# Kernel tuning notes

Measured on AMD Instinct MI355X. Metric: run time of the kernel, lower is better.

Reference implementation:

```python
import jax, jax.numpy as jnp
import numpy as np

N_NODES = 100000
N_EDGES = 1600000
D_IN = 128
D_OUT = 128
SLOPE = 0.2


def setup_inputs() -> dict:
    key = jax.random.key(0)
    k1, k2, k3, k4 = jax.random.split(key, 4)
    x = jax.random.normal(k1, (N_NODES, D_IN), dtype=jnp.float32)
    edge_index = jax.random.randint(k2, (2, N_EDGES), 0, N_NODES, dtype=jnp.int64)
    scale = 1.0 / np.sqrt(D_IN)
    W_l = jax.random.normal(k3, (D_OUT, D_IN), dtype=jnp.float32) * scale
    b_l = jnp.zeros((D_OUT,), dtype=jnp.float32)
    W_r = jax.random.normal(k4, (D_OUT, D_IN), dtype=jnp.float32) * scale
    return {"x": x, "edge_index": edge_index, "W_l": W_l, "b_l": b_l, "W_r": W_r}


def reference(x, edge_index, W_l, b_l, W_r):
    # SAGEConv with mean aggregation: out = lin_l(mean_{j in N(i)} x_j) + lin_r(x_i)
    src = edge_index[0]  # message sources (x_j)
    dst = edge_index[1]  # aggregation targets (node i)
    n = x.shape[0]
    msg = x[src]  # [E, D_IN] gather
    summed = jax.ops.segment_sum(msg, dst, num_segments=n)  # [N, D_IN]
    cnt = jax.ops.segment_sum(jnp.ones((src.shape[0],), x.dtype), dst, num_segments=n)
    agg = summed / jnp.maximum(cnt, 1.0)[:, None]  # mean; zero-degree -> 0
    out = agg @ W_l.T + b_l + x @ W_r.T  # lin_l has bias, lin_r bias=False (PyG)
    # LeakyReLU(slope); Dropout(0.5) is identity in eval mode
    return jnp.where(out > 0, out, SLOPE * out)
```

## Files before the change

kernel.cpp:

```cpp
#include <hip/hip_runtime.h>

#define D 128
#define N_SCAN 1024
#define BSH 7
#define MAXBINS 1024

typedef float  f32x4  __attribute__((ext_vector_type(4)));
typedef short  s16x8  __attribute__((ext_vector_type(8)));
typedef unsigned short us8 __attribute__((ext_vector_type(8)));

__device__ __forceinline__ unsigned short f2bf(float f) {
    unsigned b = __float_as_uint(f);
    return (unsigned short)((b + 0x7fffu + ((b >> 16) & 1u)) >> 16);
}
__device__ __forceinline__ float bf2f(unsigned short u) {
    return __uint_as_float((unsigned)u << 16);
}

__global__ __launch_bounds__(256) void bin_hist(
    const int* __restrict__ dst, int* __restrict__ bincnt, int E, int BINS)
{
    __shared__ int h[MAXBINS];
    for (int b = threadIdx.x; b < BINS; b += 256) h[b] = 0;
    __syncthreads();
    int base = blockIdx.x * 4096;
    #pragma unroll
    for (int j = 0; j < 16; ++j) {
        int e = base + j * 256 + threadIdx.x;
        if (e < E) atomicAdd(&h[dst[e] >> BSH], 1);
    }
    __syncthreads();
    for (int b = threadIdx.x; b < BINS; b += 256)
        if (h[b]) atomicAdd(&bincnt[b], h[b]);
}

__global__ __launch_bounds__(256) void bin_scan(
    const int* __restrict__ bincnt, int* __restrict__ binptr,
    int* __restrict__ binhead, int* __restrict__ rowptr,
    int BINS, int N, int E)
{
    __shared__ int sl[256];
    const int t = threadIdx.x;
    int v[4];
    int s = 0;
    #pragma unroll
    for (int j = 0; j < 4; ++j) {
        int i = t * 4 + j;
        int c = (i < BINS) ? bincnt[i] : 0;
        v[j] = s;
        s += c;
    }
    sl[t] = s;
    __syncthreads();
    for (int off = 1; off < 256; off <<= 1) {
        int add = (t >= off) ? sl[t - off] : 0;
        __syncthreads();
        sl[t] += add;
        __syncthreads();
    }
    int excl = sl[t] - s;
    #pragma unroll
    for (int j = 0; j < 4; ++j) {
        int i = t * 4 + j;
        if (i < BINS) { binptr[i] = excl + v[j]; binhead[i] = excl + v[j]; }
    }
    if (t == 0) { binptr[BINS] = E; rowptr[N] = E; }
}

__global__ __launch_bounds__(256) void partition_edges(
    const int* __restrict__ src, const int* __restrict__ dst,
    int* __restrict__ binhead, unsigned* __restrict__ packed_g, int E, int BINS)
{
    __shared__ int h[MAXBINS];
    __shared__ int goff[MAXBINS];
    __shared__ int fill[MAXBINS];
    const int t = threadIdx.x;
    for (int b = t; b < BINS; b += 256) { h[b] = 0; fill[b] = 0; }
    __syncthreads();
    int base = blockIdx.x * 4096;
    int eb[16];
    unsigned pk[16];
    #pragma unroll
    for (int j = 0; j < 16; ++j) {
        int e = base + j * 256 + t;
        if (e < E) {
            int d = dst[e], s = src[e];
            eb[j] = d >> BSH;
            pk[j] = ((unsigned)(d & ((1 << BSH) - 1)) << 17) | (unsigned)s;
            atomicAdd(&h[eb[j]], 1);
        } else eb[j] = -1;
    }
    __syncthreads();
    for (int b = t; b < BINS; b += 256)
        if (h[b]) goff[b] = atomicAdd(&binhead[b], h[b]);
    __syncthreads();
    #pragma unroll
    for (int j = 0; j < 16; ++j) {
        if (eb[j] >= 0) {
            int p = goff[eb[j]] + atomicAdd(&fill[eb[j]], 1);
            packed_g[p] = pk[j];
        }
    }
}

__global__ __launch_bounds__(256) void bin_finalize(
    const unsigned* __restrict__ packed_g, const int* __restrict__ binptr,
    int* __restrict__ rowptr, int* __restrict__ srcs, int N)
{
    const int bin = blockIdx.x, t = threadIdx.x;
    const int beg = binptr[bin], end = binptr[bin + 1];
    const int node0 = bin << BSH;
    __shared__ int c[128];
    __shared__ int pf[128];
    __shared__ int hd[128];
    if (t < 128) c[t] = 0;
    __syncthreads();
    for (int i = beg + t; i < end; i += 256)
        atomicAdd(&c[packed_g[i] >> 17], 1);
    __syncthreads();
    if (t < 128) pf[t] = c[t];
    __syncthreads();
    for (int off = 1; off < 128; off <<= 1) {
        int v = 0;
        if (t < 128 && t >= off) v = pf[t - off];
        __syncthreads();
        if (t < 128) pf[t] += v;
        __syncthreads();
    }
    if (t < 128) {
        int node = node0 + t;
        if (node < N) {
            int r = beg + pf[t] - c[t];
            rowptr[node] = r;
            hd[t] = r;
        }
    }
    __syncthreads();
    for (int i = beg + t; i < end; i += 256) {
        unsigned p = packed_g[i];
        int dl = p >> 17;
        int s = p & 0x1FFFF;
        int pos = atomicAdd(&hd[dl], 1);
        srcs[pos] = s << 8;
    }
}

__global__ __launch_bounds__(256) void hist_kernel(
    const int* __restrict__ dst, int* __restrict__ cnt, int E)
{
    int e = blockIdx.x * 256 + threadIdx.x;
    if (e < E) atomicAdd(&cnt[dst[e]], 1);
}

__global__ __launch_bounds__(256) void scan1_kernel(
    const int* __restrict__ cnt, int* __restrict__ rowptr,
    int* __restrict__ blocksum, int N)
{
    __shared__ int sl[256];
    const int t = threadIdx.x;
    const int base = blockIdx.x * N_SCAN + t * 4;
    int v[4];
    int s = 0;
    #pragma unroll
    for (int j = 0; j < 4; ++j) {
        int i = base + j;
        int c = (i < N) ? cnt[i] : 0;
        v[j] = s;
        s += c;
    }
    sl[t] = s;
    __syncthreads();
    for (int off = 1; off < 256; off <<= 1) {
        int add = (t >= off) ? sl[t - off] : 0;
        __syncthreads();
        sl[t] += add;
        __syncthreads();
    }
    int incl = sl[t];
    int excl = incl - s;
    #pragma unroll
    for (int j = 0; j < 4; ++j) {
        int i = base + j;
        if (i < N) rowptr[i] = excl + v[j];
    }
    if (t == 255) blocksum[blockIdx.x] = incl;
}

__global__ void scan2_kernel(const int* __restrict__ blocksum,
                             int* __restrict__ blockoff, int nblk)
{
    if (threadIdx.x == 0 && blockIdx.x == 0) {
        int s = 0;
        for (int b = 0; b < nblk; ++b) { blockoff[b] = s; s += blocksum[b]; }
    }
}

__global__ __launch_bounds__(256) void scan3_kernel(
    int* __restrict__ rowptr, const int* __restrict__ blockoff,
    int* __restrict__ head, int N, int E)
{
    int i = blockIdx.x * 256 + threadIdx.x;
    if (i < N) {
        int r = rowptr[i] + blockoff[i >> 10];
        rowptr[i] = r;
        head[i] = r;
    } else if (i == N) {
        rowptr[N] = E;
    }
}

__global__ __launch_bounds__(256) void scatter_edges(
    const int* __restrict__ src, const int* __restrict__ dst,
    int* __restrict__ head, int* __restrict__ srcs, int E)
{
    int e = blockIdx.x * 256 + threadIdx.x;
    if (e < E) {
        int pos = atomicAdd(&head[dst[e]], 1);
        srcs[pos] = src[e];
    }
}

__global__ __launch_bounds__(256) void convert_bf16(
    const float* __restrict__ x, unsigned short* __restrict__ xb, long long total)
{
    long long i = ((long long)blockIdx.x * 256 + threadIdx.x) * 8;
    if (i >= total) return;
    float4 f0 = *(const float4*)(x + i);
    float4 f1 = *(const float4*)(x + i + 4);
    us8 u;
    u[0] = f2bf(f0.x); u[1] = f2bf(f0.y); u[2] = f2bf(f0.z); u[3] = f2bf(f0.w);
    u[4] = f2bf(f1.x); u[5] = f2bf(f1.y); u[6] = f2bf(f1.z); u[7] = f2bf(f1.w);
    *(us8*)(xb + i) = u;
}

__global__ __launch_bounds__(256) void aggregate_row(
    const unsigned short* __restrict__ xb, const int* __restrict__ rowptr,
    const int* __restrict__ srcs, unsigned short* __restrict__ aggb, int N)
{
    int wid  = (blockIdx.x * 256 + threadIdx.x) >> 6;
    int lane = threadIdx.x & 63;
    if (wid >= N) return;
    const int beg = rowptr[wid], end = rowptr[wid + 1];
    const char* xbase = (const char*)xb;

    float accL = 0.f, accH = 0.f;
    for (int b = beg; b < end; b += 64) {
        int idx = b + lane;
        int srcv = srcs[idx < end ? idx : end - 1];
        int cnt = end - b; if (cnt > 64) cnt = 64;
        int i = 0;
        for (; i + 8 <= cnt; i += 8) {
            unsigned u[8];
            #pragma unroll
            for (int j = 0; j < 8; ++j) {
                int so = __builtin_amdgcn_readlane(srcv, i + j);
                u[j] = *(const unsigned*)(xbase + so + lane * 4);
            }
            #pragma unroll
            for (int j = 0; j < 8; ++j) {
                accL += __uint_as_float(u[j] << 16);
                accH += __uint_as_float(u[j] & 0xffff0000u);
            }
        }
        for (; i < cnt; ++i) {
            int so = __builtin_amdgcn_readlane(srcv, i);
            unsigned u = *(const unsigned*)(xbase + so + lane * 4);
            accL += __uint_as_float(u << 16);
            accH += __uint_as_float(u & 0xffff0000u);
        }
    }
    float inv = 1.0f / fmaxf((float)(end - beg), 1.0f);
    unsigned lo = f2bf(accL * inv);
    unsigned hi = f2bf(accH * inv);
    ((unsigned*)aggb)[(size_t)wid * 64 + lane] = lo | (hi << 16);
}

__global__ __launch_bounds__(256) void aggregate_bf16(
    const unsigned short* __restrict__ xb, const int* __restrict__ rowptr,
    const int* __restrict__ srcs, unsigned short* __restrict__ aggb, int N)
{
    int wid  = (blockIdx.x * 256 + threadIdx.x) >> 6;
    int lane = threadIdx.x & 63;
    if (wid >= N) return;
    int beg = rowptr[wid], end = rowptr[wid + 1];
    const int q  = lane >> 4;
    const int sl = lane & 15;

    float acc[8] = {};
    int e = beg;
    for (; e + 8 <= end; e += 8) {
        int s0 = srcs[e + q];
        int s1 = srcs[e + 4 + q];
        us8 v0 = *(const us8*)(xb + (long long)s0 * D + sl * 8);
        us8 v1 = *(const us8*)(xb + (long long)s1 * D + sl * 8);
        #pragma unroll
        for (int j = 0; j < 8; ++j) acc[j] += bf2f(v0[j]);
        #pragma unroll
        for (int j = 0; j < 8; ++j) acc[j] += bf2f(v1[j]);
    }
    for (; e < end; e += 4) {
        int ee = e + q;
        if (ee < end) {
            int s0 = srcs[ee];
            us8 v0 = *(const us8*)(xb + (long long)s0 * D + sl * 8);
            #pragma unroll
            for (int j = 0; j < 8; ++j) acc[j] += bf2f(v0[j]);
        }
    }
    #pragma unroll
    for (int j = 0; j < 8; ++j) {
        acc[j] += __shfl_xor(acc[j], 16, 64);
        acc[j] += __shfl_xor(acc[j], 32, 64);
    }
    float inv = 1.0f / fmaxf((float)(end - beg), 1.0f);
    if (q == 0) {
        us8 u;
        #pragma unroll
        for (int j = 0; j < 8; ++j) u[j] = f2bf(acc[j] * inv);
        *(us8*)(aggb + (long long)wid * D + sl * 8) = u;
    }
}

__global__ __launch_bounds__(256) void convert_w(
    const float* __restrict__ Wl, const float* __restrict__ Wr,
    unsigned short* __restrict__ wbf)
{
    int c = blockIdx.x * 256 + threadIdx.x;
    if (c >= 4096) return;
    int byte = c * 16;
    int o  = byte >> 9;
    int k2 = (byte & 511) >> 1;
    const float* srcw = (k2 < 128) ? (Wl + o * D + k2) : (Wr + o * D + (k2 - 128));
    float4 f0 = *(const float4*)(srcw);
    float4 f1 = *(const float4*)(srcw + 4);
    us8 u;
    u[0] = f2bf(f0.x); u[1] = f2bf(f0.y); u[2] = f2bf(f0.z); u[3] = f2bf(f0.w);
    u[4] = f2bf(f1.x); u[5] = f2bf(f1.y); u[6] = f2bf(f1.z); u[7] = f2bf(f1.w);
    *(us8*)((char*)wbf + (byte ^ ((o & 7) << 4))) = u;
}

__global__ __launch_bounds__(512) void mm_mfma2(
    const unsigned short* __restrict__ xb,
    const unsigned short* __restrict__ aggb,
    const unsigned short* __restrict__ wbf,
    const float* __restrict__ bl,
    float* __restrict__ out, int N)
{
    __shared__ char wlds[64 * 1024];
    const int tid = threadIdx.x;

    {
        const us8* s = (const us8*)wbf;
        us8* d = (us8*)wlds;
        #pragma unroll
        for (int j = 0; j < 8; ++j)
            d[j * 512 + tid] = s[j * 512 + tid];
    }
    __syncthreads();

    const int lane = tid & 63;
    const int wv   = tid >> 6;
    const long long m0 = (long long)blockIdx.x * 256 + wv * 32;
    const int arow = lane & 15;
    const int kq   = lane >> 4;
    const long long r0 = m0 + arow;
    const long long r1 = m0 + 16 + arow;
    const bool v0 = (r0 < N), v1 = (r1 < N);
    const unsigned short* a0 = aggb + r0 * D + kq * 8;
    const unsigned short* x0 = xb   + r0 * D + kq * 8;
    const unsigned short* a1 = aggb + r1 * D + kq * 8;
    const unsigned short* x1 = xb   + r1 * D + kq * 8;

    f32x4 acc0[8] = {};
    f32x4 acc1[8] = {};

    #pragma unroll
    for (int s = 0; s < 8; ++s) {
        s16x8 af0 = {0, 0, 0, 0, 0, 0, 0, 0};
        s16x8 af1 = {0, 0, 0, 0, 0, 0, 0, 0};
        if (v0) af0 = *(const s16x8*)((s < 4) ? (a0 + s * 32) : (x0 + (s - 4) * 32));
        if (v1) af1 = *(const s16x8*)((s < 4) ? (a1 + s * 32) : (x1 + (s - 4) * 32));
        #pragma unroll
        for (int t = 0; t < 8; ++t) {
            int o = t * 16 + arow;
            int boff = (o << 9) + s * 64 + kq * 16;
            boff ^= (o & 7) << 4;
            s16x8 bf = *(const s16x8*)(wlds + boff);
            acc0[t] = __builtin_amdgcn_mfma_f32_16x16x32_bf16(af0, bf, acc0[t], 0, 0, 0);
            acc1[t] = __builtin_amdgcn_mfma_f32_16x16x32_bf16(af1, bf, acc1[t], 0, 0, 0);
        }
    }

    const int crow = (lane >> 4) * 4;
    const int ccol = lane & 15;
    #pragma unroll
    for (int t = 0; t < 8; ++t) {
        int col = t * 16 + ccol;
        float bb = bl[col];
        #pragma unroll
        for (int r = 0; r < 4; ++r) {
            long long row0 = m0 + crow + r;
            if (row0 < N) {
                float vv = acc0[t][r] + bb;
                out[row0 * D + col] = vv > 0.f ? vv : 0.2f * vv;
            }
            long long row1 = m0 + 16 + crow + r;
            if (row1 < N) {
                float vv = acc1[t][r] + bb;
                out[row1 * D + col] = vv > 0.f ? vv : 0.2f * vv;
            }
        }
    }
}

__global__ __launch_bounds__(256) void mm_mfma(
    const unsigned short* __restrict__ xb,
    const unsigned short* __restrict__ aggb,
    const float* __restrict__ Wl, const float* __restrict__ bl,
    const float* __restrict__ Wr,
    float* __restrict__ out, int N)
{
    __shared__ char wlds[64 * 1024];
    const int tid = threadIdx.x;

    for (int c = tid; c < 4096; c += 256) {
        int byte = c * 16;
        int o  = byte >> 9;
        int k2 = (byte & 511) >> 1;
        const float* srcw = (k2 < 128) ? (Wl + o * D + k2) : (Wr + o * D + (k2 - 128));
        float4 f0 = *(const float4*)(srcw);
        float4 f1 = *(const float4*)(srcw + 4);
        us8 u;
        u[0] = f2bf(f0.x); u[1] = f2bf(f0.y); u[2] = f2bf(f0.z); u[3] = f2bf(f0.w);
        u[4] = f2bf(f1.x); u[5] = f2bf(f1.y); u[6] = f2bf(f1.z); u[7] = f2bf(f1.w);
        *(us8*)(wlds + (byte ^ ((o & 7) << 4))) = u;
    }
    __syncthreads();

    const int lane = tid & 63;
    const int wv   = tid >> 6;
    const long long m0 = (long long)blockIdx.x * 64 + wv * 16;
    const int arow = lane & 15;
    const int kq   = lane >> 4;
    const long long mrow = m0 + arow;
    const bool valid = (mrow < N);
    const unsigned short* aP = aggb + mrow * D + kq * 8;
    const unsigned short* xP = xb   + mrow * D + kq * 8;

    f32x4 acc[8] = {};

    #pragma unroll
    for (int s = 0; s < 8; ++s) {
        s16x8 afrag = {0, 0, 0, 0, 0, 0, 0, 0};
        if (valid) {
            const unsigned short* ap = (s < 4) ? (aP + s * 32) : (xP + (s - 4) * 32);
            afrag = *(const s16x8*)ap;
        }
        #pragma unroll
        for (int t = 0; t < 8; ++t) {
            int o = t * 16 + arow;
            int boff = (o << 9) + s * 64 + kq * 16;
            boff ^= (o & 7) << 4;
            s16x8 bfrag = *(const s16x8*)(wlds + boff);
            acc[t] = __builtin_amdgcn_mfma_f32_16x16x32_bf16(afrag, bfrag, acc[t], 0, 0, 0);
        }
    }

    const int crow = (lane >> 4) * 4;
    const int ccol = lane & 15;
    #pragma unroll
    for (int t = 0; t < 8; ++t) {
        int col = t * 16 + ccol;
        float bb = bl[col];
        #pragma unroll
        for (int r = 0; r < 4; ++r) {
            long long row = m0 + crow + r;
            if (row < N) {
                float v = acc[t][r] + bb;
                out[row * D + col] = v > 0.f ? v : 0.2f * v;
            }
        }
    }
}

__global__ __launch_bounds__(256) void aggregate_f32(
    const float* __restrict__ x, const int* __restrict__ rowptr,
    const int* __restrict__ srcs, float* __restrict__ out, int N)
{
    int wid  = (blockIdx.x * 256 + threadIdx.x) >> 6;
    int lane = threadIdx.x & 63;
    if (wid >= N) return;
    int beg = rowptr[wid], end = rowptr[wid + 1];
    const float2* x2 = (const float2*)x;
    float ax = 0.f, ay = 0.f;
    int e = beg;
    for (; e + 4 <= end; e += 4) {
        int s0 = srcs[e], s1 = srcs[e + 1], s2 = srcs[e + 2], s3 = srcs[e + 3];
        float2 v0 = x2[(long long)s0 * 64 + lane];
        float2 v1 = x2[(long long)s1 * 64 + lane];
        float2 v2 = x2[(long long)s2 * 64 + lane];
        float2 v3 = x2[(long long)s3 * 64 + lane];
        ax += v0.x + v1.x + v2.x + v3.x;
        ay += v0.y + v1.y + v2.y + v3.y;
    }
    for (; e < end; ++e) {
        float2 v = x2[(long long)srcs[e] * 64 + lane];
        ax += v.x; ay += v.y;
    }
    float inv = 1.0f / fmaxf((float)(end - beg), 1.0f);
    float2 o; o.x = ax * inv; o.y = ay * inv;
    ((float2*)out)[(long long)wid * 64 + lane] = o;
}

#define MT 32
#define KT 32
__global__ __launch_bounds__(256) void sage_mm_f32(
    const float* __restrict__ x, const float* __restrict__ Wl,
    const float* __restrict__ bl, const float* __restrict__ Wr,
    float* __restrict__ out, int N)
{
    __shared__ __align__(16) float a_s[KT][MT + 4];
    __shared__ __align__(16) float x_s[KT][MT + 4];
    __shared__ __align__(16) float wl_s[KT][D + 4];
    __shared__ __align__(16) float wr_s[KT][D + 4];

    const int tid = threadIdx.x;
    const int tx = tid & 31;
    const int ty = tid >> 5;
    const int node0 = blockIdx.x * MT;

    float acc[4][4] = {};

    for (int k0 = 0; k0 < D; k0 += KT) {
        __syncthreads();
        for (int i = tid; i < MT * KT; i += 256) {
            int n = i >> 5, kk = i & 31;
            int node = node0 + n;
            float av = 0.f, xv = 0.f;
            if (node < N) {
                av = out[(long long)node * D + k0 + kk];
                xv = x[(long long)node * D + k0 + kk];
            }
            a_s[kk][n] = av;
            x_s[kk][n] = xv;
        }
        for (int i = tid; i < D * KT; i += 256) {
            int o = i >> 5, kk = i & 31;
            wl_s[kk][o] = Wl[o * D + k0 + kk];
            wr_s[kk][o] = Wr[o * D + k0 + kk];
        }
        __syncthreads();
        #pragma unroll
        for (int kk = 0; kk < KT; ++kk) {
            float4 a4 = *(const float4*)&a_s[kk][ty * 4];
            float4 x4 = *(const float4*)&x_s[kk][ty * 4];
            float4 l4 = *(const float4*)&wl_s[kk][tx * 4];
            float4 r4 = *(const float4*)&wr_s[kk][tx * 4];
            float an[4] = {a4.x, a4.y, a4.z, a4.w};
            float xn[4] = {x4.x, x4.y, x4.z, x4.w};
            float lo[4] = {l4.x, l4.y, l4.z, l4.w};
            float ro[4] = {r4.x, r4.y, r4.z, r4.w};
            #pragma unroll
            for (int n = 0; n < 4; ++n)
                #pragma unroll
                for (int o = 0; o < 4; ++o)
                    acc[n][o] += an[n] * lo[o] + xn[n] * ro[o];
        }
    }

    float4 b4 = *(const float4*)&bl[tx * 4];
    float bb[4] = {b4.x, b4.y, b4.z, b4.w};
    #pragma unroll
    for (int n = 0; n < 4; ++n) {
        int node = node0 + ty * 4 + n;
        if (node < N) {
            float4 o4;
            float* po = (float*)&o4;
            #pragma unroll
            for (int o = 0; o < 4; ++o) {
                float v = acc[n][o] + bb[o];
                po[o] = v > 0.f ? v : 0.2f * v;
            }
            *(float4*)&out[(long long)node * D + tx * 4] = o4;
        }
    }
}

extern "C" void kernel_launch(void* const* d_in, const int* in_sizes, int n_in,
                              void* d_out, int out_size, void* d_ws, size_t ws_size,
                              hipStream_t stream)
{
    const float* x  = (const float*)d_in[0];
    const int*   ei = (const int*)d_in[1];
    const float* Wl = (const float*)d_in[2];
    const float* bl = (const float*)d_in[3];
    const float* Wr = (const float*)d_in[4];

    const int E = in_sizes[1] / 2;
    const int N = out_size / D;
    const int* src = ei;
    const int* dst = ei + E;
    float* out = (float*)d_out;
    const int BINS = (N + (1 << BSH) - 1) >> BSH;

    size_t off = 0;
    auto take = [&](size_t bytes) { size_t p = off; off = (off + bytes + 255) & ~(size_t)255; return p; };
    char* w = (char*)d_ws;
    int* rowptr   = (int*)(w + take((size_t)(N + 1) * 4));
    int* srcs     = (int*)(w + take((size_t)E * 4));
    int* bincnt   = (int*)(w + take((size_t)BINS * 4));
    int* binptr   = (int*)(w + take((size_t)(BINS + 1) * 4));
    int* binhead  = (int*)(w + take((size_t)BINS * 4));
    unsigned* packed = (unsigned*)(w + take((size_t)E * 4));
    unsigned short* wbf = (unsigned short*)(w + take(64 * 1024));
    unsigned short* xbf   = (unsigned short*)(w + take((size_t)N * D * 2));
    unsigned short* aggbf = (unsigned short*)(w + take((size_t)N * D * 2));
    size_t full_needed = off;

    const bool binned_ok = (BINS <= MAXBINS) && (N < (1 << 17)) && (ws_size >= full_needed);

    if (binned_ok) {
        convert_w<<<16, 256, 0, stream>>>(Wl, Wr, wbf);

        hipMemsetAsync(bincnt, 0, (size_t)BINS * 4, stream);
        int pb = (E + 4095) / 4096;
        bin_hist<<<pb, 256, 0, stream>>>(dst, bincnt, E, BINS);
        bin_scan<<<1, 256, 0, stream>>>(bincnt, binptr, binhead, rowptr, BINS, N, E);
        partition_edges<<<pb, 256, 0, stream>>>(src, dst, binhead, packed, E, BINS);
        bin_finalize<<<BINS, 256, 0, stream>>>(packed, binptr, rowptr, srcs, N);

        long long total = (long long)N * D;
        int cb = (int)((total / 8 + 255) / 256);
        convert_bf16<<<cb, 256, 0, stream>>>(x, xbf, total);
        int ab = (N * 64 + 255) / 256;
        aggregate_row<<<ab, 256, 0, stream>>>(xbf, rowptr, srcs, aggbf, N);
        int mb = (N + 255) / 256;
        mm_mfma2<<<mb, 512, 0, stream>>>(xbf, aggbf, wbf, bl, out, N);
        return;
    }

    off = 0;
    int* cnt    = (int*)(w + take((size_t)N * 4));
    rowptr      = (int*)(w + take((size_t)(N + 1) * 4));
    int* head   = (int*)(w + take((size_t)N * 4));
    int* blocksum = (int*)(w + take(4096));
    int* blockoff = (int*)(w + take(4096));
    srcs        = (int*)(w + take((size_t)E * 4));
    size_t base_needed = off;
    xbf   = (unsigned short*)(w + take((size_t)N * D * 2));
    aggbf = (unsigned short*)(w + take((size_t)N * D * 2));
    size_t bf16_needed = off;

    hipMemsetAsync(cnt, 0, (size_t)N * 4, stream);
    const int eb = (E + 255) / 256;
    hist_kernel<<<eb, 256, 0, stream>>>(dst, cnt, E);
    const int nblk = (N + N_SCAN - 1) / N_SCAN;
    scan1_kernel<<<nblk, 256, 0, stream>>>(cnt, rowptr, blocksum, N);
    scan2_kernel<<<1, 64, 0, stream>>>(blocksum, blockoff, nblk);
    scan3_kernel<<<(N + 1 + 255) / 256, 256, 0, stream>>>(rowptr, blockoff, head, N, E);
    scatter_edges<<<eb, 256, 0, stream>>>(src, dst, head, srcs, E);

    if (ws_size >= bf16_needed) {
        long long total = (long long)N * D;
        int cb = (int)((total / 8 + 255) / 256);
        convert_bf16<<<cb, 256, 0, stream>>>(x, xbf, total);
        int ab = (N * 64 + 255) / 256;
        aggregate_bf16<<<ab, 256, 0, stream>>>(xbf, rowptr, srcs, aggbf, N);
        int mb = (N + 63) / 64;
        mm_mfma<<<mb, 256, 0, stream>>>(xbf, aggbf, Wl, bl, Wr, out, N);
    } else {
        (void)base_needed;
        int ab = (N * 64 + 255) / 256;
        aggregate_f32<<<ab, 256, 0, stream>>>(x, rowptr, srcs, out, N);
        sage_mm_f32<<<(N + MT - 1) / MT, 256, 0, stream>>>(x, Wl, bl, Wr, out, N);
    }
}
```

Before: 166.1 us.

## Pre-swizzle weights into MFMA fragment order and read B from global instead of LDS

```diff
diff --git a/kernel.cpp b/kernel.cpp
--- a/kernel.cpp
+++ b/kernel.cpp
@@ -321,46 +321,37 @@
     }
 }
 
-__global__ __launch_bounds__(256) void convert_w(
+__global__ __launch_bounds__(256) void convert_w_frag(
     const float* __restrict__ Wl, const float* __restrict__ Wr,
     unsigned short* __restrict__ wbf)
 {
     int c = blockIdx.x * 256 + threadIdx.x;
     if (c >= 4096) return;
-    int byte = c * 16;
-    int o  = byte >> 9;
-    int k2 = (byte & 511) >> 1;
+    int l  = c & 63;
+    int ts = c >> 6;
+    int t  = ts >> 3, s = ts & 7;
+    int o  = t * 16 + (l & 15);
+    int k2 = s * 32 + (l >> 4) * 8;
     const float* srcw = (k2 < 128) ? (Wl + o * D + k2) : (Wr + o * D + (k2 - 128));
     float4 f0 = *(const float4*)(srcw);
     float4 f1 = *(const float4*)(srcw + 4);
     us8 u;
     u[0] = f2bf(f0.x); u[1] = f2bf(f0.y); u[2] = f2bf(f0.z); u[3] = f2bf(f0.w);
     u[4] = f2bf(f1.x); u[5] = f2bf(f1.y); u[6] = f2bf(f1.z); u[7] = f2bf(f1.w);
-    *(us8*)((char*)wbf + (byte ^ ((o & 7) << 4))) = u;
-}
-
-__global__ __launch_bounds__(512) void mm_mfma2(
+    ((us8*)wbf)[c] = u;
+}
+
+__global__ __launch_bounds__(256) void mm_mfma3(
     const unsigned short* __restrict__ xb,
     const unsigned short* __restrict__ aggb,
-    const unsigned short* __restrict__ wbf,
+    const unsigned short* __restrict__ wfrag,
     const float* __restrict__ bl,
     float* __restrict__ out, int N)
 {
-    __shared__ char wlds[64 * 1024];
-    const int tid = threadIdx.x;
-
-    {
-        const us8* s = (const us8*)wbf;
-        us8* d = (us8*)wlds;
-        #pragma unroll
-        for (int j = 0; j < 8; ++j)
-            d[j * 512 + tid] = s[j * 512 + tid];
-    }
-    __syncthreads();
-
+    const int tid  = threadIdx.x;
     const int lane = tid & 63;
     const int wv   = tid >> 6;
-    const long long m0 = (long long)blockIdx.x * 256 + wv * 32;
+    const long long m0 = (long long)blockIdx.x * 128 + wv * 32;
     const int arow = lane & 15;
     const int kq   = lane >> 4;
     const long long r0 = m0 + arow;
@@ -370,6 +361,7 @@
     const unsigned short* x0 = xb   + r0 * D + kq * 8;
     const unsigned short* a1 = aggb + r1 * D + kq * 8;
     const unsigned short* x1 = xb   + r1 * D + kq * 8;
+    const s16x8* wf = (const s16x8*)wfrag;
 
     f32x4 acc0[8] = {};
     f32x4 acc1[8] = {};
@@ -382,10 +374,7 @@
         if (v1) af1 = *(const s16x8*)((s < 4) ? (a1 + s * 32) : (x1 + (s - 4) * 32));
         #pragma unroll
         for (int t = 0; t < 8; ++t) {
-            int o = t * 16 + arow;
-            int boff = (o << 9) + s * 64 + kq * 16;
-            boff ^= (o & 7) << 4;
-            s16x8 bf = *(const s16x8*)(wlds + boff);
+            s16x8 bf = wf[(t * 8 + s) * 64 + lane];
             acc0[t] = __builtin_amdgcn_mfma_f32_16x16x32_bf16(af0, bf, acc0[t], 0, 0, 0);
             acc1[t] = __builtin_amdgcn_mfma_f32_16x16x32_bf16(af1, bf, acc1[t], 0, 0, 0);
         }
@@ -620,7 +609,7 @@
     const bool binned_ok = (BINS <= MAXBINS) && (N < (1 << 17)) && (ws_size >= full_needed);
 
     if (binned_ok) {
-        convert_w<<<16, 256, 0, stream>>>(Wl, Wr, wbf);
+        convert_w_frag<<<16, 256, 0, stream>>>(Wl, Wr, wbf);
 
         hipMemsetAsync(bincnt, 0, (size_t)BINS * 4, stream);
         int pb = (E + 4095) / 4096;
@@ -634,8 +623,8 @@
         convert_bf16<<<cb, 256, 0, stream>>>(x, xbf, total);
         int ab = (N * 64 + 255) / 256;
         aggregate_row<<<ab, 256, 0, stream>>>(xbf, rowptr, srcs, aggbf, N);
-        int mb = (N + 255) / 256;
-        mm_mfma2<<<mb, 512, 0, stream>>>(xbf, aggbf, wbf, bl, out, N);
+        int mb = (N + 127) / 128;
+        mm_mfma3<<<mb, 256, 0, stream>>>(xbf, aggbf, wbf, bl, out, N);
         return;
     }
 
```

Result: slower. 181.2 us (+9.1%).
